# Kernel tuning notes

Measured on AMD Instinct MI355X. Metric: run time of the kernel, lower is better.

## Reference

```python
import jax, jax.numpy as jnp
import numpy as np

N = 100000      # nodes
E = 1600000     # edges per adjacency
NFEAT = 128
NHID = 128


def _digcn_conv(x, w, b, src, dst, edge_attr, num_nodes):
    # x @ W, then gather source, scale by edge weight, scatter-add to dst (PyG add-aggr)
    h = x @ w                                   # [N, out]
    msg = edge_attr[:, None] * h[src]           # [E, out]
    out = jax.ops.segment_sum(msg, dst, num_segments=num_nodes)
    return out + b


def _inception(x, ln_w, ln_b, c1_w, c1_b, c2_w, c2_b,
               edge_index, edge_attr, edge_index2, edge_attr2):
    x0 = x @ ln_w + ln_b
    x1 = _digcn_conv(x, c1_w, c1_b, edge_index[0], edge_index[1], edge_attr, x.shape[0])
    x2 = _digcn_conv(x, c2_w, c2_b, edge_index2[0], edge_index2[1], edge_attr2, x.shape[0])
    # eval mode: dropout is identity; the module sums the three branches
    return x0 + x1 + x2


def _mk_params(key, dims):
    ps = {}
    blocks = [("b1", NFEAT, NHID), ("b2", NHID, NHID), ("b3", NHID, NHID)]
    for name, din, dout in blocks:
        for pfx in ("ln", "c1", "c2"):
            key, k1 = jax.random.split(key)
            ps[f"{name}_{pfx}_w"] = jax.random.normal(k1, (din, dout), jnp.float32) * (1.0 / np.sqrt(din))
            ps[f"{name}_{pfx}_b"] = jnp.zeros((dout,), jnp.float32)
    return ps


def setup_inputs() -> dict:
    key = jax.random.key(0)
    ks = jax.random.split(key, 8)
    inp = {
        "x": jax.random.normal(ks[0], (N, NFEAT), jnp.float32),
        "edge_index": jax.random.randint(ks[1], (2, E), 0, N, jnp.int64 if jax.config.jax_enable_x64 else jnp.int32).astype(jnp.int32),
        "edge_attr": jax.random.uniform(ks[2], (E,), jnp.float32),
        "edge_index2": jax.random.randint(ks[3], (2, E), 0, N).astype(jnp.int32),
        "edge_attr2": jax.random.uniform(ks[4], (E,), jnp.float32),
    }
    inp.update(_mk_params(ks[5], None))
    return inp


def reference(x, edge_index, edge_attr, edge_index2, edge_attr2,
              b1_ln_w, b1_ln_b, b1_c1_w, b1_c1_b, b1_c2_w, b1_c2_b,
              b2_ln_w, b2_ln_b, b2_c1_w, b2_c1_b, b2_c2_w, b2_c2_b,
              b3_ln_w, b3_ln_b, b3_c1_w, b3_c1_b, b3_c2_w, b3_c2_b):
    x = _inception(x, b1_ln_w, b1_ln_b, b1_c1_w, b1_c1_b, b1_c2_w, b1_c2_b,
                   edge_index, edge_attr, edge_index2, edge_attr2)
    x = _inception(x, b2_ln_w, b2_ln_b, b2_c1_w, b2_c1_b, b2_c2_w, b2_c2_b,
                   edge_index, edge_attr, edge_index2, edge_attr2)
    x = _inception(x, b3_ln_w, b3_ln_b, b3_c1_w, b3_c1_b, b3_c2_w, b3_c2_b,
                   edge_index, edge_attr, edge_index2, edge_attr2)
    # torch module splits x per-graph via data.batch (data-dependent shapes);
    # we return the full node embedding matrix [N, NHID] instead.
    return x
```

## Files before the change

### kernel.cpp

```cpp
#include <hip/hip_runtime.h>
#include <hip/hip_bf16.h>

#define DIM 128
#define CHUNK 8192
#define NBK 256
#define BSHIFT 10

typedef __attribute__((ext_vector_type(8))) short bf16x8;
typedef __attribute__((ext_vector_type(4))) float f32x4;
typedef __attribute__((ext_vector_type(2))) unsigned u32x2;

static __device__ __forceinline__ short f2bf(float f) {
    union { float f; unsigned u; } v; v.f = f;
    unsigned r = (v.u + 0x7FFF + ((v.u >> 16) & 1)) >> 16;
    return (short)r;
}
static __device__ __forceinline__ float asf(unsigned u) {
    union { unsigned u; float f; } v; v.u = u; return v.f;
}
static __device__ __forceinline__ unsigned asu(float f) {
    union { float f; unsigned u; } v; v.f = f; return v.u;
}

struct WPtrs { const float* w[9]; };
__global__ __launch_bounds__(256) void prep_w_k(WPtrs p, short* __restrict__ wt)
{
    const int g = blockIdx.x * 256 + threadIdx.x;
    if (g >= 9 * 8 * 4 * 64) return;
    const int lane = g & 63;
    const int ks   = (g >> 6) & 3;
    const int ctl  = (g >> 8) & 7;
    const int mat  = g >> 11;
    const int layer = mat / 3;
    const int matl  = mat % 3;
    const int n     = ctl * 16 + (lane & 15);
    const int kbase = ks * 32 + (lane >> 4) * 8;
    const float* W = p.w[mat];
    short o[8];
#pragma unroll
    for (int j = 0; j < 8; ++j) o[j] = f2bf(W[(size_t)(kbase + j) * DIM + n]);
    short* dst = wt + (size_t)layer * 49152
                    + ((size_t)(ks * 24 + matl * 8 + ctl) << 9) + lane * 8;
#pragma unroll
    for (int j = 0; j < 8; ++j) dst[j] = o[j];
}

__global__ __launch_bounds__(256) void mfma_gemm_k(
    const float* __restrict__ X, const short* __restrict__ Wp,
    const float* __restrict__ b0, const float* __restrict__ b1,
    const float* __restrict__ b2,
    float* __restrict__ Y, short* __restrict__ H1, short* __restrict__ H2,
    int N)
{
    __shared__ __align__(16) short As[64][DIM + 8];
    __shared__ __align__(16) short Bs[24 * 512];
    const int t  = threadIdx.x;
    const int m0 = blockIdx.x * 64;

    for (int idx = t; idx < 64 * 32; idx += 256) {
        const int r  = idx >> 5;
        const int c4 = (idx & 31) << 2;
        float4 v = make_float4(0.f, 0.f, 0.f, 0.f);
        if (m0 + r < N) v = *(const float4*)(X + (size_t)(m0 + r) * DIM + c4);
        short4 s;
        s.x = f2bf(v.x); s.y = f2bf(v.y); s.z = f2bf(v.z); s.w = f2bf(v.w);
        *(short4*)&As[r][c4] = s;
    }
    __syncthreads();

    const int wave  = t >> 6;
    const int lane  = t & 63;
    const int l15   = lane & 15;
    const int kq    = lane >> 4;
    const int mbase = wave * 16;

    bf16x8 afr[4];
#pragma unroll
    for (int ks = 0; ks < 4; ++ks)
        afr[ks] = *(const bf16x8*)&As[mbase + l15][ks * 32 + kq * 8];

    f32x4 acc[24];
#pragma unroll
    for (int ct = 0; ct < 24; ++ct) acc[ct] = (f32x4){0.f, 0.f, 0.f, 0.f};

    for (int ks = 0; ks < 4; ++ks) {
        if (ks) __syncthreads();
        const uint4* wsrc = (const uint4*)(Wp + ks * 12288);
#pragma unroll
        for (int i = 0; i < 6; ++i)
            ((uint4*)Bs)[t + i * 256] = wsrc[t + i * 256];
        __syncthreads();

        const bf16x8 a = afr[ks];
#pragma unroll
        for (int ct = 0; ct < 24; ++ct) {
            const bf16x8 b = *(const bf16x8*)&Bs[ct * 512 + lane * 8];
            acc[ct] = __builtin_amdgcn_mfma_f32_16x16x32_bf16(a, b, acc[ct], 0, 0, 0);
        }
    }

#pragma unroll
    for (int ct = 0; ct < 24; ++ct) {
        const int col = ct * 16 + l15;
        float bias = 0.f;
        if (col < DIM) bias = b0[col] + b1[col] + b2[col];
#pragma unroll
        for (int r = 0; r < 4; ++r) {
            const int m = m0 + mbase + kq * 4 + r;
            if (m >= N) continue;
            const float v = acc[ct][r];
            if (col < DIM)            Y [(size_t)m * DIM + col]             = v + bias;
            else if (col < 2 * DIM)   H1[(size_t)m * DIM + (col - DIM)]     = f2bf(v);
            else                      H2[(size_t)m * DIM + (col - 2 * DIM)] = f2bf(v);
        }
    }
}


__global__ __launch_bounds__(256) void p0_bhist_k(
    const int* __restrict__ d1, const int* __restrict__ d2,
    int* __restrict__ bcnt, int N, int E, int E2)
{
    __shared__ int lh[NBK];
    const int t = threadIdx.x;
    lh[t] = 0;
    __syncthreads();
    const int stride = gridDim.x * 256;
    for (int i = blockIdx.x * 256 + t; i < E;  i += stride) atomicAdd(&lh[d1[i] >> BSHIFT], 1);
    for (int i = blockIdx.x * 256 + t; i < E2; i += stride) atomicAdd(&lh[(N + d2[i]) >> BSHIFT], 1);
    __syncthreads();
    if (lh[t]) atomicAdd(&bcnt[t], lh[t]);
}

__global__ __launch_bounds__(256) void bscan_k(
    const int* __restrict__ bcnt, int* __restrict__ bktbase,
    int* __restrict__ cursor, int* __restrict__ rowptr, int twoN, int ET)
{
    __shared__ int sv[NBK];
    const int t = threadIdx.x;
    sv[t] = bcnt[t];
    __syncthreads();
    for (int off = 1; off < NBK; off <<= 1) {
        int a = (t >= off) ? sv[t - off] : 0;
        __syncthreads();
        sv[t] += a;
        __syncthreads();
    }
    const int excl = t ? sv[t - 1] : 0;
    bktbase[t] = excl;
    cursor[t]  = excl;
    if (t == 0) rowptr[twoN] = ET;
}

__global__ __launch_bounds__(256) void p1_bin_k(
    const int* __restrict__ s1, const int* __restrict__ d1, const float* __restrict__ ea1,
    const int* __restrict__ s2, const int* __restrict__ d2, const float* __restrict__ ea2,
    int* __restrict__ cursor, uint2* __restrict__ binned,
    int N, int E, int E2, int nc1)
{
    __shared__ __align__(16) uint2 stage[CHUNK];
    __shared__ unsigned char lbkt[CHUNK];
    __shared__ int hist[NBK], exclv[NBK], lcur[NBK], gpos[NBK];

    const int t = threadIdx.x;
    const int c = blockIdx.x;
    const bool a2 = (c >= nc1);
    const int* S  = a2 ? s2  : s1;
    const int* D  = a2 ? d2  : d1;
    const float* W = a2 ? ea2 : ea1;
    const int Eloc = a2 ? E2 : E;
    const int voff = a2 ? N : 0;
    const int eb   = (a2 ? (c - nc1) : c) * CHUNK;
    const int ec   = min(CHUNK, Eloc - eb);

    hist[t] = 0;
    __syncthreads();

    for (int i = t; i < ec; i += 256)
        atomicAdd(&hist[(unsigned)(voff + D[eb + i]) >> BSHIFT], 1);
    __syncthreads();

    exclv[t] = hist[t];
    __syncthreads();
    for (int off = 1; off < NBK; off <<= 1) {
        int a = (t >= off) ? exclv[t - off] : 0;
        __syncthreads();
        exclv[t] += a;
        __syncthreads();
    }
    const int myincl = exclv[t];
    __syncthreads();
    exclv[t] = myincl - hist[t];
    lcur[t]  = exclv[t];
    if (hist[t]) gpos[t] = atomicAdd(&cursor[t], hist[t]);
    __syncthreads();

    for (int i = t; i < ec; i += 256) {
        const int v = voff + D[eb + i];
        const int b = (unsigned)v >> BSHIFT;
        const int lpos = atomicAdd(&lcur[b], 1);
        stage[lpos] = make_uint2((unsigned)S[eb + i] | ((unsigned)(v & 1023) << 17),
                                 asu(W[eb + i]));
        lbkt[lpos] = (unsigned char)b;
    }
    __syncthreads();

    for (int s = t; s < ec; s += 256) {
        const int b = lbkt[s];
        binned[gpos[b] + (s - exclv[b])] = stage[s];
    }
}

__global__ __launch_bounds__(256) void p2_final_k(
    const uint2* __restrict__ binned, const int* __restrict__ bktbase,
    int* __restrict__ rowptr, uint2* __restrict__ pairs, int twoN)
{
    __shared__ int hist[1024], scn[1024], lcur[1024];
    const int t = threadIdx.x;
    const int b = blockIdx.x;
    const int base = bktbase[b];
    const int cnt  = bktbase[b + 1] - base;
    const int vbase = b << BSHIFT;

    for (int i = t; i < 1024; i += 256) hist[i] = 0;
    __syncthreads();

    for (int i = t; i < cnt; i += 256)
        atomicAdd(&hist[binned[base + i].x >> 17], 1);
    __syncthreads();

    for (int i = t; i < 1024; i += 256) scn[i] = hist[i];
    __syncthreads();
    for (int off = 1; off < 1024; off <<= 1) {
        int a0 = (t       >= off) ? scn[t       - off] : 0;
        int a1 = (t + 256 >= off) ? scn[t + 256 - off] : 0;
        int a2 = (t + 512 >= off) ? scn[t + 512 - off] : 0;
        int a3 = (t + 768 >= off) ? scn[t + 768 - off] : 0;
        __syncthreads();
        scn[t] += a0; scn[t + 256] += a1; scn[t + 512] += a2; scn[t + 768] += a3;
        __syncthreads();
    }
    for (int i = t; i < 1024; i += 256) {
        const int excl = scn[i] - hist[i];
        lcur[i] = excl;
        const int v = vbase + i;
        if (v < twoN) rowptr[v] = base + excl;
    }
    __syncthreads();

    for (int i = t; i < cnt; i += 256) {
        const uint2 e = binned[base + i];
        const int vlow = e.x >> 17;
        const int pos = base + atomicAdd(&lcur[vlow], 1);
        pairs[pos] = make_uint2(e.x & 0x1FFFFu, e.y);
    }
}

static __device__ __forceinline__ void bf2acc(unsigned w, uint2 h, f32x4& acc)
{
    const float wf = asf(w);
    acc.x = fmaf(wf, asf(h.x << 16), acc.x);
    acc.y = fmaf(wf, asf(h.x & 0xFFFF0000u), acc.y);
    acc.z = fmaf(wf, asf(h.y << 16), acc.z);
    acc.w = fmaf(wf, asf(h.y & 0xFFFF0000u), acc.w);
}

static __device__ __forceinline__ void gacc(
    const short* __restrict__ H, const uint2* __restrict__ pairs,
    int start, int end, int lane, f32x4& acc)
{
    int j = start;
    for (; j + 7 < end; j += 8) {
        u32x2 p[8]; uint2 h[8];
#pragma unroll
        for (int q = 0; q < 8; ++q)
            p[q] = __builtin_nontemporal_load((const u32x2*)(pairs + j + q));
#pragma unroll
        for (int q = 0; q < 8; ++q)
            h[q] = *(const uint2*)(H + (size_t)p[q].x * DIM + lane * 4);
#pragma unroll
        for (int q = 0; q < 8; ++q) bf2acc(p[q].y, h[q], acc);
    }
    if (j + 3 < end) {
        u32x2 p[4]; uint2 h[4];
#pragma unroll
        for (int q = 0; q < 4; ++q)
            p[q] = __builtin_nontemporal_load((const u32x2*)(pairs + j + q));
#pragma unroll
        for (int q = 0; q < 4; ++q)
            h[q] = *(const uint2*)(H + (size_t)p[q].x * DIM + lane * 4);
#pragma unroll
        for (int q = 0; q < 4; ++q) bf2acc(p[q].y, h[q], acc);
        j += 4;
    }
    for (; j < end; ++j) {
        const u32x2 p = __builtin_nontemporal_load((const u32x2*)(pairs + j));
        const uint2 h = *(const uint2*)(H + (size_t)p.x * DIM + lane * 4);
        bf2acc(p.y, h, acc);
    }
}

__global__ __launch_bounds__(256) void gather2_k(
    const short* __restrict__ H1, const short* __restrict__ H2,
    const uint2* __restrict__ pairs, const int* __restrict__ rowptr,
    float* __restrict__ Y, int N)
{
    const int node = blockIdx.x * 8 + (threadIdx.x >> 5);
    if (node >= N) return;
    const int lane = threadIdx.x & 31;

    const int s1 = rowptr[node];
    const int e1 = rowptr[node + 1];
    const int s2 = rowptr[N + node];
    const int e2 = rowptr[N + node + 1];

    f32x4 acc = (f32x4){0.f, 0.f, 0.f, 0.f};
    gacc(H1, pairs, s1, e1, lane, acc);
    gacc(H2, pairs, s2, e2, lane, acc);

    f32x4* yp = (f32x4*)(Y + (size_t)node * DIM + lane * 4);
    f32x4 y = __builtin_nontemporal_load(yp);
    y += acc;
    __builtin_nontemporal_store(y, yp);
}

extern "C" void kernel_launch(void* const* d_in, const int* in_sizes, int n_in,
                              void* d_out, int out_size, void* d_ws, size_t ws_size,
                              hipStream_t stream)
{
    const float* x   = (const float*)d_in[0];
    const int*   ei  = (const int*)d_in[1];
    const float* ea  = (const float*)d_in[2];
    const int*   ei2 = (const int*)d_in[3];
    const float* ea2 = (const float*)d_in[4];

    const int N  = in_sizes[0] / DIM;
    const int E  = in_sizes[2];
    const int E2 = in_sizes[4];
    const int ET = E + E2;

    float* OUT = (float*)d_out;

    float* B      = (float*)d_ws;
    short* H1     = (short*)(B + (size_t)N * DIM);
    short* H2     = H1 + (size_t)N * DIM;
    short* WT     = H2 + (size_t)N * DIM;
    int*   rowptr = (int*)(WT + 9 * 16384);
    int*   bcnt   = rowptr + 2 * N + 4;
    int*   bktbase= bcnt + NBK;
    int*   cursor = bktbase + NBK + 4;
    uint2* pairs  = (uint2*)(cursor + NBK);
    uint2* binned = (uint2*)B;

    WPtrs wp;
    for (int b = 0; b < 3; ++b) {
        wp.w[b * 3 + 0] = (const float*)d_in[5 + 6 * b + 0];
        wp.w[b * 3 + 1] = (const float*)d_in[5 + 6 * b + 2];
        wp.w[b * 3 + 2] = (const float*)d_in[5 + 6 * b + 4];
    }
    prep_w_k<<<(18432 + 255) / 256, 256, 0, stream>>>(wp, WT);

    const int nc1 = (E + CHUNK - 1) / CHUNK;
    const int nc2 = (E2 + CHUNK - 1) / CHUNK;
    const int nbk_used = (2 * N + (1 << BSHIFT) - 1) >> BSHIFT;

    hipMemsetAsync(bcnt, 0, NBK * sizeof(int), stream);
    p0_bhist_k<<<256, 256, 0, stream>>>(ei + E, ei2 + E2, bcnt, N, E, E2);
    bscan_k<<<1, NBK, 0, stream>>>(bcnt, bktbase, cursor, rowptr, 2 * N, ET);
    p1_bin_k<<<nc1 + nc2, 256, 0, stream>>>(ei, ei + E, ea, ei2, ei2 + E2, ea2,
                                            cursor, binned, N, E, E2, nc1);
    p2_final_k<<<nbk_used, 256, 0, stream>>>(binned, bktbase, rowptr, pairs, 2 * N);

    const int gGemm   = (N + 63) / 64;
    const int gGather = (N + 7) / 8;

    const float* cur = x;
    for (int b = 0; b < 3; ++b) {
        const float* lnb = (const float*)d_in[5 + 6 * b + 1];
        const float* c1b = (const float*)d_in[5 + 6 * b + 3];
        const float* c2b = (const float*)d_in[5 + 6 * b + 5];

        float* y = (b == 1) ? B : OUT;

        mfma_gemm_k<<<gGemm, 256, 0, stream>>>(
            cur, WT + (size_t)b * 49152, lnb, c1b, c2b, y, H1, H2, N);

        gather2_k<<<gGather, 256, 0, stream>>>(H1, H2, pairs, rowptr, y, N);

        cur = y;
    }
}
```

Baseline: 867.6 us.

## Aggregate first then transform: gather on bf16 X, single K=384 GEMM

Reorders each layer so the sparse aggregation runs on the bf16 input features (A·X) before the dense transform, writing G1/G2 in bf16. A single GEMM with K=384 then computes [X|G1|G2]·[Wln;Wc1;Wc2] plus bias, which removes the read-modify-write of fp32 Y in the gather and the separate H1/H2 bf16 outputs. Intermediate layer activations are kept in bf16 and the input is cast once up front. The aggregated sums are rounded to bf16 before the GEMM, and activations between layers also lose precision.

```diff
diff --git a/kernel.cpp b/kernel.cpp
--- a/kernel.cpp
+++ b/kernel.cpp
@@ -1,5 +1,4 @@
 #include <hip/hip_runtime.h>
-#include <hip/hip_bf16.h>
 
 #define DIM 128
 #define CHUNK 8192
@@ -21,50 +20,66 @@
 static __device__ __forceinline__ unsigned asu(float f) {
     union { float f; unsigned u; } v; v.f = f; return v.u;
 }
+static __device__ __forceinline__ unsigned pk2(float a, float b) {
+    return (unsigned)(unsigned short)f2bf(a) | ((unsigned)(unsigned short)f2bf(b) << 16);
+}
 
 struct WPtrs { const float* w[9]; };
 __global__ __launch_bounds__(256) void prep_w_k(WPtrs p, short* __restrict__ wt)
 {
     const int g = blockIdx.x * 256 + threadIdx.x;
-    if (g >= 9 * 8 * 4 * 64) return;
+    if (g >= 3 * 12 * 8 * 64) return;
     const int lane = g & 63;
-    const int ks   = (g >> 6) & 3;
-    const int ctl  = (g >> 8) & 7;
-    const int mat  = g >> 11;
-    const int layer = mat / 3;
-    const int matl  = mat % 3;
-    const int n     = ctl * 16 + (lane & 15);
-    const int kbase = ks * 32 + (lane >> 4) * 8;
-    const float* W = p.w[mat];
-    short o[8];
-#pragma unroll
-    for (int j = 0; j < 8; ++j) o[j] = f2bf(W[(size_t)(kbase + j) * DIM + n]);
-    short* dst = wt + (size_t)layer * 49152
-                    + ((size_t)(ks * 24 + matl * 8 + ctl) << 9) + lane * 8;
-#pragma unroll
-    for (int j = 0; j < 8; ++j) dst[j] = o[j];
+    const int ct   = (g >> 6) & 7;
+    const int rest = g >> 9;
+    const int ks   = rest % 12;
+    const int layer = rest / 12;
+    const int mat   = ks >> 2;
+    const int n     = ct * 16 + (lane & 15);
+    const int kbase = (ks & 3) * 32 + (lane >> 4) * 8;
+    const float* W = p.w[layer * 3 + mat];
+    short* dst = wt + (size_t)layer * 49152 + ks * 4096 + ct * 512 + lane * 8;
+#pragma unroll
+    for (int j = 0; j < 8; ++j) dst[j] = f2bf(W[(size_t)(kbase + j) * DIM + n]);
+}
+
+__global__ __launch_bounds__(256) void cast_k(
+    const float* __restrict__ X, short* __restrict__ Xb, int n8)
+{
+    const int i = blockIdx.x * 256 + threadIdx.x;
+    if (i >= n8) return;
+    const float4* xp = (const float4*)X + (size_t)i * 2;
+    const float4 a = xp[0];
+    const float4 b = xp[1];
+    bf16x8 v;
+    v[0] = f2bf(a.x); v[1] = f2bf(a.y); v[2] = f2bf(a.z); v[3] = f2bf(a.w);
+    v[4] = f2bf(b.x); v[5] = f2bf(b.y); v[6] = f2bf(b.z); v[7] = f2bf(b.w);
+    *(bf16x8*)(Xb + (size_t)i * 8) = v;
 }
 
 __global__ __launch_bounds__(256) void mfma_gemm_k(
-    const float* __restrict__ X, const short* __restrict__ Wp,
+    const short* __restrict__ Xb, const short* __restrict__ G1,
+    const short* __restrict__ G2, const short* __restrict__ Wp,
     const float* __restrict__ b0, const float* __restrict__ b1,
     const float* __restrict__ b2,
-    float* __restrict__ Y, short* __restrict__ H1, short* __restrict__ H2,
-    int N)
-{
-    __shared__ __align__(16) short As[64][DIM + 8];
-    __shared__ __align__(16) short Bs[24 * 512];
+    float* __restrict__ Yf, short* __restrict__ Yb, int N)
+{
+    __shared__ __align__(16) short As[64][384 + 8];
+    __shared__ __align__(16) short Bs[4096];
     const int t  = threadIdx.x;
     const int m0 = blockIdx.x * 64;
 
-    for (int idx = t; idx < 64 * 32; idx += 256) {
-        const int r  = idx >> 5;
-        const int c4 = (idx & 31) << 2;
-        float4 v = make_float4(0.f, 0.f, 0.f, 0.f);
-        if (m0 + r < N) v = *(const float4*)(X + (size_t)(m0 + r) * DIM + c4);
-        short4 s;
-        s.x = f2bf(v.x); s.y = f2bf(v.y); s.z = f2bf(v.z); s.w = f2bf(v.w);
-        *(short4*)&As[r][c4] = s;
+    for (int idx = t; idx < 64 * 48; idx += 256) {
+        const int r = idx / 48;
+        const int c = (idx % 48) * 8;
+        bf16x8 v = (bf16x8){0,0,0,0,0,0,0,0};
+        if (m0 + r < N) {
+            const short* src = (c < 128) ? (Xb + (size_t)(m0 + r) * DIM + c)
+                             : (c < 256) ? (G1 + (size_t)(m0 + r) * DIM + (c - 128))
+                                         : (G2 + (size_t)(m0 + r) * DIM + (c - 256));
+            v = *(const bf16x8*)src;
+        }
+        *(bf16x8*)&As[r][c] = v;
     }
     __syncthreads();
 
@@ -74,44 +89,42 @@
     const int kq    = lane >> 4;
     const int mbase = wave * 16;
 
-    bf16x8 afr[4];
-#pragma unroll
-    for (int ks = 0; ks < 4; ++ks)
+    bf16x8 afr[12];
+#pragma unroll
+    for (int ks = 0; ks < 12; ++ks)
         afr[ks] = *(const bf16x8*)&As[mbase + l15][ks * 32 + kq * 8];
 
-    f32x4 acc[24];
-#pragma unroll
-    for (int ct = 0; ct < 24; ++ct) acc[ct] = (f32x4){0.f, 0.f, 0.f, 0.f};
-
-    for (int ks = 0; ks < 4; ++ks) {
+    f32x4 acc[8];
+#pragma unroll
+    for (int ct = 0; ct < 8; ++ct) acc[ct] = (f32x4){0.f, 0.f, 0.f, 0.f};
+
+#pragma unroll
+    for (int ks = 0; ks < 12; ++ks) {
         if (ks) __syncthreads();
-        const uint4* wsrc = (const uint4*)(Wp + ks * 12288);
-#pragma unroll
-        for (int i = 0; i < 6; ++i)
-            ((uint4*)Bs)[t + i * 256] = wsrc[t + i * 256];
+        const uint4* wsrc = (const uint4*)(Wp + ks * 4096);
+        ((uint4*)Bs)[t]       = wsrc[t];
+        ((uint4*)Bs)[t + 256] = wsrc[t + 256];
         __syncthreads();
 
         const bf16x8 a = afr[ks];
 #pragma unroll
-        for (int ct = 0; ct < 24; ++ct) {
+        for (int ct = 0; ct < 8; ++ct) {
             const bf16x8 b = *(const bf16x8*)&Bs[ct * 512 + lane * 8];
             acc[ct] = __builtin_amdgcn_mfma_f32_16x16x32_bf16(a, b, acc[ct], 0, 0, 0);
         }
     }
 
 #pragma unroll
-    for (int ct = 0; ct < 24; ++ct) {
+    for (int ct = 0; ct < 8; ++ct) {
         const int col = ct * 16 + l15;
-        float bias = 0.f;
-        if (col < DIM) bias = b0[col] + b1[col] + b2[col];
+        const float bias = b0[col] + b1[col] + b2[col];
 #pragma unroll
         for (int r = 0; r < 4; ++r) {
             const int m = m0 + mbase + kq * 4 + r;
             if (m >= N) continue;
-            const float v = acc[ct][r];
-            if (col < DIM)            Y [(size_t)m * DIM + col]             = v + bias;
-            else if (col < 2 * DIM)   H1[(size_t)m * DIM + (col - DIM)]     = f2bf(v);
-            else                      H2[(size_t)m * DIM + (col - 2 * DIM)] = f2bf(v);
+            const float v = acc[ct][r] + bias;
+            if (Yf) Yf[(size_t)m * DIM + col] = v;
+            else    Yb[(size_t)m * DIM + col] = f2bf(v);
         }
     }
 }
@@ -300,10 +313,10 @@
     }
 }
 
-__global__ __launch_bounds__(256) void gather2_k(
-    const short* __restrict__ H1, const short* __restrict__ H2,
+__global__ __launch_bounds__(256) void gatherX_k(
+    const short* __restrict__ Xb,
     const uint2* __restrict__ pairs, const int* __restrict__ rowptr,
-    float* __restrict__ Y, int N)
+    short* __restrict__ G1, short* __restrict__ G2, int N)
 {
     const int node = blockIdx.x * 8 + (threadIdx.x >> 5);
     if (node >= N) return;
@@ -314,14 +327,14 @@
     const int s2 = rowptr[N + node];
     const int e2 = rowptr[N + node + 1];
 
-    f32x4 acc = (f32x4){0.f, 0.f, 0.f, 0.f};
-    gacc(H1, pairs, s1, e1, lane, acc);
-    gacc(H2, pairs, s2, e2, lane, acc);
-
-    f32x4* yp = (f32x4*)(Y + (size_t)node * DIM + lane * 4);
-    f32x4 y = __builtin_nontemporal_load(yp);
-    y += acc;
-    __builtin_nontemporal_store(y, yp);
+    f32x4 a1 = (f32x4){0.f, 0.f, 0.f, 0.f};
+    f32x4 a2 = (f32x4){0.f, 0.f, 0.f, 0.f};
+    gacc(Xb, pairs, s1, e1, lane, a1);
+    gacc(Xb, pairs, s2, e2, lane, a2);
+
+    const size_t off = (size_t)node * DIM + lane * 4;
+    *(uint2*)(G1 + off) = make_uint2(pk2(a1.x, a1.y), pk2(a1.z, a1.w));
+    *(uint2*)(G2 + off) = make_uint2(pk2(a2.x, a2.y), pk2(a2.z, a2.w));
 }
 
 extern "C" void kernel_launch(void* const* d_in, const int* in_sizes, int n_in,
@@ -341,16 +354,17 @@
 
     float* OUT = (float*)d_out;
 
-    float* B      = (float*)d_ws;
-    short* H1     = (short*)(B + (size_t)N * DIM);
-    short* H2     = H1 + (size_t)N * DIM;
-    short* WT     = H2 + (size_t)N * DIM;
-    int*   rowptr = (int*)(WT + 9 * 16384);
+    short* Xb0 = (short*)d_ws;
+    short* Xb1 = Xb0 + (size_t)N * DIM;
+    short* G1  = Xb1 + (size_t)N * DIM;
+    short* G2  = G1  + (size_t)N * DIM;
+    short* WT  = G2  + (size_t)N * DIM;
+    int*   rowptr = (int*)(WT + 3 * 49152);
     int*   bcnt   = rowptr + 2 * N + 4;
     int*   bktbase= bcnt + NBK;
     int*   cursor = bktbase + NBK + 4;
     uint2* pairs  = (uint2*)(cursor + NBK);
-    uint2* binned = (uint2*)B;
+    uint2* binned = (uint2*)G1;
 
     WPtrs wp;
     for (int b = 0; b < 3; ++b) {
@@ -359,6 +373,9 @@
         wp.w[b * 3 + 2] = (const float*)d_in[5 + 6 * b + 4];
     }
     prep_w_k<<<(18432 + 255) / 256, 256, 0, stream>>>(wp, WT);
+
+    const int n8 = N * DIM / 8;
+    cast_k<<<(n8 + 255) / 256, 256, 0, stream>>>(x, Xb0, n8);
 
     const int nc1 = (E + CHUNK - 1) / CHUNK;
     const int nc2 = (E2 + CHUNK - 1) / CHUNK;
@@ -374,19 +391,20 @@
     const int gGemm   = (N + 63) / 64;
     const int gGather = (N + 7) / 8;
 
-    const float* cur = x;
+    const short* cur = Xb0;
     for (int b = 0; b < 3; ++b) {
         const float* lnb = (const float*)d_in[5 + 6 * b + 1];
         const float* c1b = (const float*)d_in[5 + 6 * b + 3];
         const float* c2b = (const float*)d_in[5 + 6 * b + 5];
 
-        float* y = (b == 1) ? B : OUT;
+        gatherX_k<<<gGather, 256, 0, stream>>>(cur, pairs, rowptr, G1, G2, N);
+
+        float* yf = (b == 2) ? OUT : nullptr;
+        short* yb = (b == 2) ? nullptr : ((cur == Xb0) ? Xb1 : Xb0);
 
         mfma_gemm_k<<<gGemm, 256, 0, stream>>>(
-            cur, WT + (size_t)b * 49152, lnb, c1b, c2b, y, H1, H2, N);
-
-        gather2_k<<<gGather, 256, 0, stream>>>(H1, H2, pairs, rowptr, y, N);
-
-        cur = y;
-    }
-}
+            cur, G1, G2, WT + (size_t)b * 49152, lnb, c1b, c2b, yf, yb, N);
+
+        if (b < 2) cur = yb;
+    }
+}
```

New measurement: 858.4 us. Within noise of the previous version (-1.1%).
